# Kernel optimization log

Measured on AMD Instinct MI355X. Metric: run time of the kernel, lower is better.

## Reference

```python
import jax, jax.numpy as jnp
import numpy as np

TEMPERATURE = 8.0  # sqrt(head_dim=64)
MASK_FILL = -1e9


def setup_inputs() -> dict:
    key = jax.random.key(0)
    kq, kk, kv, km = jax.random.split(key, 4)
    B, H, S, D = 4, 16, 2048, 64
    q = jax.random.normal(kq, (B, H, S, D), dtype=jnp.float32)
    k = jax.random.normal(kk, (B, H, S, D), dtype=jnp.float32)
    v = jax.random.normal(kv, (B, H, S, D), dtype=jnp.float32)
    mask = jax.random.randint(km, (B, 1, S, S), 0, 2).astype(bool)
    return {"q": q, "k": k, "v": v, "mask": mask}


def reference(q, k, v, mask):
    # scores: [B,H,S,S]
    attn = jnp.einsum('bhqd,bhkd->bhqk', q / TEMPERATURE, k)
    attn = jnp.where(mask, MASK_FILL, attn)
    attn = jax.nn.softmax(attn, axis=-1)  # dropout in eval mode = identity
    out = jnp.einsum('bhqk,bhkd->bhqd', attn, v)
    return (out, attn)
```

## Files before the change

kernel.cpp:

```cpp
#include <hip/hip_runtime.h>
#include <math.h>


#define SEQ 2048
#define HD 64
#define NH 16
#define NB 4

typedef float floatx4 __attribute__((ext_vector_type(4)));
typedef __bf16 bf16x8 __attribute__((ext_vector_type(8)));

__device__ __forceinline__ void split8(const float4 a, const float4 b, const float s,
                                       bf16x8& hi, bf16x8& lo) {
  float f[8] = {a.x * s, a.y * s, a.z * s, a.w * s,
                b.x * s, b.y * s, b.z * s, b.w * s};
#pragma unroll
  for (int j = 0; j < 8; ++j) {
    __bf16 h = (__bf16)f[j];
    hi[j] = h;
    lo[j] = (__bf16)(f[j] - (float)h);
  }
}

__global__ __launch_bounds__(256, 2) void sdpa_kernel(
    const float* __restrict__ qp, const float* __restrict__ kp,
    const float* __restrict__ vp, const int* __restrict__ maskp,
    float* __restrict__ outp) {
  const int tid  = threadIdx.x;
  const int lane = tid & 63;
  const int w    = tid >> 6;
  const int ll   = lane & 15;
  const int quad = lane >> 4;
  const int q0   = blockIdx.x * 16;
  const int bh   = blockIdx.y;
  const int b    = bh >> 4;

  __shared__ __align__(16) __bf16 vT[64][264];
  __shared__ __align__(16) __bf16 pC[16][264];
  __shared__ float red_m[4][16];
  __shared__ float red_l[4][16];

  const size_t bh_off = (size_t)bh * (SEQ * HD);

  bf16x8 qhi0, qlo0, qhi1, qlo1;
  {
    const float* qr = qp + bh_off + (size_t)(q0 + ll) * HD + quad * 8;
    float4 a0 = *(const float4*)(qr);
    float4 a1 = *(const float4*)(qr + 4);
    float4 a2 = *(const float4*)(qr + 32);
    float4 a3 = *(const float4*)(qr + 36);
    split8(a0, a1, 0.125f, qhi0, qlo0);
    split8(a2, a3, 0.125f, qhi1, qlo1);
  }

  floatx4 acc[32];
#pragma unroll
  for (int i = 0; i < 32; ++i) acc[i] = 0.f;

  const float* kb = kp + bh_off;
#pragma unroll
  for (int i = 0; i < 32; ++i) {
    const int col0 = (4 * i + w) * 16;
    const float* kr = kb + (size_t)(col0 + ll) * HD + quad * 8;
    float4 a0 = *(const float4*)(kr);
    float4 a1 = *(const float4*)(kr + 4);
    float4 a2 = *(const float4*)(kr + 32);
    float4 a3 = *(const float4*)(kr + 36);
    bf16x8 khi0, klo0, khi1, klo1;
    split8(a0, a1, 1.f, khi0, klo0);
    split8(a2, a3, 1.f, khi1, klo1);
    floatx4 t = acc[i];
    t = __builtin_amdgcn_mfma_f32_16x16x32_bf16(qhi0, khi0, t, 0, 0, 0);
    t = __builtin_amdgcn_mfma_f32_16x16x32_bf16(qlo0, khi0, t, 0, 0, 0);
    t = __builtin_amdgcn_mfma_f32_16x16x32_bf16(qhi0, klo0, t, 0, 0, 0);
    t = __builtin_amdgcn_mfma_f32_16x16x32_bf16(qhi1, khi1, t, 0, 0, 0);
    t = __builtin_amdgcn_mfma_f32_16x16x32_bf16(qlo1, khi1, t, 0, 0, 0);
    t = __builtin_amdgcn_mfma_f32_16x16x32_bf16(qhi1, klo1, t, 0, 0, 0);
    acc[i] = t;
  }

  const int* mb = maskp + (size_t)b * SEQ * SEQ;
  float mx[4] = {-INFINITY, -INFINITY, -INFINITY, -INFINITY};
#pragma unroll
  for (int i = 0; i < 32; ++i) {
    const int col = (4 * i + w) * 16 + ll;
#pragma unroll
    for (int r = 0; r < 4; ++r) {
      const int row = q0 + quad * 4 + r;
      const int mv = mb[(size_t)row * SEQ + col];
      float sv = mv ? -1e9f : acc[i][r];
      acc[i][r] = sv;
      mx[r] = fmaxf(mx[r], sv);
    }
  }
#pragma unroll
  for (int d = 1; d < 16; d <<= 1) {
#pragma unroll
    for (int r = 0; r < 4; ++r) mx[r] = fmaxf(mx[r], __shfl_xor(mx[r], d, 64));
  }
  if (ll == 0) {
#pragma unroll
    for (int r = 0; r < 4; ++r) red_m[w][quad * 4 + r] = mx[r];
  }
  __syncthreads();
  float mrow[4];
#pragma unroll
  for (int r = 0; r < 4; ++r) {
    const int row = quad * 4 + r;
    mrow[r] = fmaxf(fmaxf(red_m[0][row], red_m[1][row]),
                    fmaxf(red_m[2][row], red_m[3][row]));
  }

  float sm[4] = {0.f, 0.f, 0.f, 0.f};
#pragma unroll
  for (int i = 0; i < 32; ++i) {
#pragma unroll
    for (int r = 0; r < 4; ++r) {
      float e = __expf(acc[i][r] - mrow[r]);
      acc[i][r] = e;
      sm[r] += e;
    }
  }
#pragma unroll
  for (int d = 1; d < 16; d <<= 1) {
#pragma unroll
    for (int r = 0; r < 4; ++r) sm[r] += __shfl_xor(sm[r], d, 64);
  }
  if (ll == 0) {
#pragma unroll
    for (int r = 0; r < 4; ++r) red_l[w][quad * 4 + r] = sm[r];
  }
  __syncthreads();
  float linv[4];
#pragma unroll
  for (int r = 0; r < 4; ++r) {
    const int row = quad * 4 + r;
    linv[r] = 1.0f / (red_l[0][row] + red_l[1][row] + red_l[2][row] + red_l[3][row]);
  }

  float* attn = outp + (size_t)(NB * NH * SEQ * HD) + (size_t)bh * SEQ * SEQ;
#pragma unroll
  for (int i = 0; i < 32; ++i) {
    const int col = (4 * i + w) * 16 + ll;
#pragma unroll
    for (int r = 0; r < 4; ++r) {
      const int row = q0 + quad * 4 + r;
      float p = acc[i][r] * linv[r];
      acc[i][r] = p;
      attn[(size_t)row * SEQ + col] = p;
    }
  }

  floatx4 oacc = 0.f;
  const float* vb = vp + bh_off;
#pragma unroll
  for (int c = 0; c < 8; ++c) {
    {
      const float* vr = vb + (size_t)(c * 256 + tid) * HD;
#pragma unroll
      for (int d4 = 0; d4 < 16; ++d4) {
        float4 vv = *(const float4*)(vr + d4 * 4);
        vT[d4 * 4 + 0][tid] = (__bf16)vv.x;
        vT[d4 * 4 + 1][tid] = (__bf16)vv.y;
        vT[d4 * 4 + 2][tid] = (__bf16)vv.z;
        vT[d4 * 4 + 3][tid] = (__bf16)vv.w;
      }
    }
#pragma unroll
    for (int u = 0; u < 4; ++u) {
      const int lt = w + 4 * u;
#pragma unroll
      for (int r = 0; r < 4; ++r)
        pC[quad * 4 + r][lt * 16 + ll] = (__bf16)acc[4 * c + u][r];
    }
    __syncthreads();
#pragma unroll
    for (int kk = 0; kk < 8; ++kk) {
      bf16x8 af = *(const bf16x8*)&pC[ll][kk * 32 + quad * 8];
      bf16x8 bf = *(const bf16x8*)&vT[w * 16 + ll][kk * 32 + quad * 8];
      oacc = __builtin_amdgcn_mfma_f32_16x16x32_bf16(af, bf, oacc, 0, 0, 0);
    }
    __syncthreads();
  }

  float* ob = outp + bh_off + (size_t)q0 * HD;
#pragma unroll
  for (int r = 0; r < 4; ++r)
    ob[(size_t)(quad * 4 + r) * HD + w * 16 + ll] = oacc[r];
}

extern "C" void kernel_launch(void* const* d_in, const int* in_sizes, int n_in,
                              void* d_out, int out_size, void* d_ws, size_t ws_size,
                              hipStream_t stream) {
  const float* q = (const float*)d_in[0];
  const float* k = (const float*)d_in[1];
  const float* v = (const float*)d_in[2];
  const int* mask = (const int*)d_in[3];
  float* out = (float*)d_out;
  dim3 grid(SEQ / 16, NB * NH);
  sdpa_kernel<<<grid, dim3(256), 0, stream>>>(q, k, v, mask, out);
}
```

Before: 2.230 ms.

## Precompute split-bf16 K, transposed V and bitpacked mask in workspace, two-pass softmax

Adds prep kernels that split K into bf16 hi/lo halves, transpose V to bf16 in workspace, and pack the int mask into bit words. The main kernel then runs an online max/sum pass and a second pass that recomputes QK, writes the attention probabilities with nontemporal stores and feeds them into the PV MFMAs through lane shuffles instead of LDS. The intent is to stop every query block from re-converting K/V and re-reading the 16M-int mask. The cost is three extra launches, double the QK compute, and a fallback path when the workspace is too small.

```diff
diff --git a/kernel.cpp b/kernel.cpp
--- a/kernel.cpp
+++ b/kernel.cpp
@@ -6,6 +6,11 @@
 #define HD 64
 #define NH 16
 #define NB 4
+#define BHN (NB * NH)
+#define KN ((size_t)BHN * SEQ * HD)
+#define MASK_FILL -1e9f
+#define QSCALE (0.125f * 1.44269504088896f)
+#define WS_REQUIRED (3 * KN * sizeof(__bf16) + (size_t)NB * 64 * SEQ * sizeof(unsigned))
 
 typedef float floatx4 __attribute__((ext_vector_type(4)));
 typedef __bf16 bf16x8 __attribute__((ext_vector_type(8)));
@@ -22,7 +27,245 @@
   }
 }
 
-__global__ __launch_bounds__(256, 2) void sdpa_kernel(
+__device__ __forceinline__ unsigned pkbf(float a, float b) {
+  union { __bf16 h[2]; unsigned u; } x;
+  x.h[0] = (__bf16)a;
+  x.h[1] = (__bf16)b;
+  return x.u;
+}
+
+
+__global__ void prep_splitk(const float* __restrict__ kp, __bf16* __restrict__ khi,
+                            __bf16* __restrict__ klo) {
+  size_t i = ((size_t)blockIdx.x * 256 + threadIdx.x) * 8;
+  float4 a = *(const float4*)(kp + i);
+  float4 b = *(const float4*)(kp + i + 4);
+  bf16x8 hi, lo;
+  float f[8] = {a.x, a.y, a.z, a.w, b.x, b.y, b.z, b.w};
+#pragma unroll
+  for (int j = 0; j < 8; ++j) {
+    __bf16 h = (__bf16)f[j];
+    hi[j] = h;
+    lo[j] = (__bf16)(f[j] - (float)h);
+  }
+  *(bf16x8*)(khi + i) = hi;
+  *(bf16x8*)(klo + i) = lo;
+}
+
+__global__ void prep_vt(const float* __restrict__ vp, __bf16* __restrict__ vT) {
+  __shared__ __bf16 tile[64][72];
+  const int bhi = blockIdx.x >> 5;
+  const int s0 = (blockIdx.x & 31) * 64;
+  const int t = threadIdx.x;
+  const float* vb = vp + (size_t)bhi * SEQ * HD + (size_t)s0 * HD;
+#pragma unroll
+  for (int c = 0; c < 4; ++c) {
+    int ft = c * 256 + t;
+    int sl = ft >> 4, d0 = (ft & 15) * 4;
+    float4 x = *(const float4*)(vb + (size_t)sl * HD + d0);
+    tile[sl][d0 + 0] = (__bf16)x.x;
+    tile[sl][d0 + 1] = (__bf16)x.y;
+    tile[sl][d0 + 2] = (__bf16)x.z;
+    tile[sl][d0 + 3] = (__bf16)x.w;
+  }
+  __syncthreads();
+  const int d = t >> 2, sc = (t & 3) * 16;
+  __bf16* o = vT + (size_t)bhi * HD * SEQ + (size_t)d * SEQ + s0 + sc;
+  bf16x8 v0, v1;
+#pragma unroll
+  for (int j = 0; j < 8; ++j) {
+    v0[j] = tile[sc + j][d];
+    v1[j] = tile[sc + 8 + j][d];
+  }
+  *(bf16x8*)o = v0;
+  *(bf16x8*)(o + 8) = v1;
+}
+
+__global__ void prep_mask(const int* __restrict__ mp, unsigned* __restrict__ mbT) {
+  const int lane = threadIdx.x & 63;
+  const int w = threadIdx.x >> 6;
+  const size_t g0 = ((size_t)blockIdx.x * 4 + w) * 64;
+  unsigned long long bits = __ballot(mp[g0 + lane] != 0);
+  if (lane == 0) {
+    const int b = (int)(g0 / ((size_t)SEQ * SEQ));
+    const size_t rem = g0 % ((size_t)SEQ * SEQ);
+    const int row = (int)(rem / SEQ);
+    const int c = (int)(rem % SEQ) >> 5;
+    mbT[((size_t)b * 64 + c) * SEQ + row] = (unsigned)bits;
+    mbT[((size_t)b * 64 + c + 1) * SEQ + row] = (unsigned)(bits >> 32);
+  }
+}
+
+
+struct TileOut { unsigned d0, d1; };
+
+__device__ __forceinline__ TileOut do_tile(const __bf16* __restrict__ kh,
+                                           const __bf16* __restrict__ kl,
+                                           bf16x8 qhi0, bf16x8 qlo0, bf16x8 qhi1,
+                                           bf16x8 qlo1, unsigned bits4, float mf,
+                                           float linv, float* attn_addr) {
+  bf16x8 kh0 = *(const bf16x8*)kh, kh1 = *(const bf16x8*)(kh + 32);
+  bf16x8 kl0 = *(const bf16x8*)kl, kl1 = *(const bf16x8*)(kl + 32);
+  floatx4 a = 0.f;
+  a = __builtin_amdgcn_mfma_f32_16x16x32_bf16(kh0, qhi0, a, 0, 0, 0);
+  a = __builtin_amdgcn_mfma_f32_16x16x32_bf16(kl0, qhi0, a, 0, 0, 0);
+  a = __builtin_amdgcn_mfma_f32_16x16x32_bf16(kh0, qlo0, a, 0, 0, 0);
+  a = __builtin_amdgcn_mfma_f32_16x16x32_bf16(kh1, qhi1, a, 0, 0, 0);
+  a = __builtin_amdgcn_mfma_f32_16x16x32_bf16(kl1, qhi1, a, 0, 0, 0);
+  a = __builtin_amdgcn_mfma_f32_16x16x32_bf16(kh1, qlo1, a, 0, 0, 0);
+  float s0 = (bits4 & 1u) ? MASK_FILL : a[0];
+  float s1 = (bits4 & 2u) ? MASK_FILL : a[1];
+  float s2 = (bits4 & 4u) ? MASK_FILL : a[2];
+  float s3 = (bits4 & 8u) ? MASK_FILL : a[3];
+  float p0 = exp2f(s0 - mf) * linv;
+  float p1 = exp2f(s1 - mf) * linv;
+  float p2 = exp2f(s2 - mf) * linv;
+  float p3 = exp2f(s3 - mf) * linv;
+  floatx4 st = {p0, p1, p2, p3};
+  __builtin_nontemporal_store(st, (floatx4*)attn_addr);
+  TileOut o;
+  o.d0 = pkbf(p0, p1);
+  o.d1 = pkbf(p2, p3);
+  return o;
+}
+
+__global__ __launch_bounds__(256, 4) void sdpa_main(
+    const float* __restrict__ qp, const __bf16* __restrict__ khi,
+    const __bf16* __restrict__ klo, const __bf16* __restrict__ vT,
+    const unsigned* __restrict__ mbT, float* __restrict__ outp) {
+  const int tid = threadIdx.x;
+  const int lane = tid & 63;
+  const int w = tid >> 6;
+  const int ll = lane & 15;
+  const int quad = lane >> 4;
+  const int q0 = blockIdx.x * 16;
+  const int bh = blockIdx.y;
+  const int b = bh >> 4;
+
+  __shared__ float red_m[4][16];
+  __shared__ float red_l[4][16];
+  __shared__ float outred[4][64][17];
+
+  const size_t bh_off = (size_t)bh * (SEQ * HD);
+
+  bf16x8 qhi0, qlo0, qhi1, qlo1;
+  {
+    const float* qr = qp + bh_off + (size_t)(q0 + ll) * HD + quad * 8;
+    split8(*(const float4*)(qr), *(const float4*)(qr + 4), QSCALE, qhi0, qlo0);
+    split8(*(const float4*)(qr + 32), *(const float4*)(qr + 36), QSCALE, qhi1, qlo1);
+  }
+
+  const unsigned* mrow = mbT + (size_t)b * 64 * SEQ + (q0 + ll);
+
+  float m = -INFINITY, l = 0.f;
+#pragma unroll 4
+  for (int i = 0; i < 32; ++i) {
+    const int t = w * 32 + i;
+    const size_t kb = bh_off + (size_t)(t * 16 + ll) * HD + quad * 8;
+    bf16x8 kh0 = *(const bf16x8*)(khi + kb), kh1 = *(const bf16x8*)(khi + kb + 32);
+    bf16x8 kl0 = *(const bf16x8*)(klo + kb), kl1 = *(const bf16x8*)(klo + kb + 32);
+    floatx4 a = 0.f;
+    a = __builtin_amdgcn_mfma_f32_16x16x32_bf16(kh0, qhi0, a, 0, 0, 0);
+    a = __builtin_amdgcn_mfma_f32_16x16x32_bf16(kl0, qhi0, a, 0, 0, 0);
+    a = __builtin_amdgcn_mfma_f32_16x16x32_bf16(kh0, qlo0, a, 0, 0, 0);
+    a = __builtin_amdgcn_mfma_f32_16x16x32_bf16(kh1, qhi1, a, 0, 0, 0);
+    a = __builtin_amdgcn_mfma_f32_16x16x32_bf16(kl1, qhi1, a, 0, 0, 0);
+    a = __builtin_amdgcn_mfma_f32_16x16x32_bf16(kh1, qlo1, a, 0, 0, 0);
+    const unsigned bits = mrow[(size_t)(t >> 1) * SEQ] >> ((t & 1) * 16 + quad * 4);
+    float s0 = (bits & 1u) ? MASK_FILL : a[0];
+    float s1 = (bits & 2u) ? MASK_FILL : a[1];
+    float s2 = (bits & 4u) ? MASK_FILL : a[2];
+    float s3 = (bits & 8u) ? MASK_FILL : a[3];
+    float tm = fmaxf(fmaxf(s0, s1), fmaxf(s2, s3));
+    float mn = fmaxf(m, tm);
+    l = l * exp2f(m - mn) +
+        ((exp2f(s0 - mn) + exp2f(s1 - mn)) + (exp2f(s2 - mn) + exp2f(s3 - mn)));
+    m = mn;
+  }
+#pragma unroll
+  for (int d = 16; d <= 32; d <<= 1) {
+    float mo = __shfl_xor(m, d, 64);
+    float lo_ = __shfl_xor(l, d, 64);
+    float mn = fmaxf(m, mo);
+    l = l * exp2f(m - mn) + lo_ * exp2f(mo - mn);
+    m = mn;
+  }
+  if (lane < 16) {
+    red_m[w][lane] = m;
+    red_l[w][lane] = l;
+  }
+  __syncthreads();
+  float mf = fmaxf(fmaxf(red_m[0][ll], red_m[1][ll]),
+                   fmaxf(red_m[2][ll], red_m[3][ll]));
+  float lf = red_l[0][ll] * exp2f(red_m[0][ll] - mf) +
+             red_l[1][ll] * exp2f(red_m[1][ll] - mf) +
+             red_l[2][ll] * exp2f(red_m[2][ll] - mf) +
+             red_l[3][ll] * exp2f(red_m[3][ll] - mf);
+  const float linv = 1.0f / lf;
+
+  floatx4 o0 = 0.f, o1 = 0.f, o2 = 0.f, o3 = 0.f;
+  float* attnrow = outp + (size_t)(BHN * SEQ * HD) + (size_t)bh * SEQ * SEQ +
+                   (size_t)(q0 + ll) * SEQ;
+  const __bf16* vb = vT + (size_t)bh * HD * SEQ;
+  for (int i2 = 0; i2 < 16; ++i2) {
+    const int tA = w * 32 + 2 * i2;
+    const int j0 = tA * 16;
+    const unsigned bits = mrow[(size_t)(tA >> 1) * SEQ];
+    const size_t kbA = bh_off + (size_t)(tA * 16 + ll) * HD + quad * 8;
+    const size_t kbB = kbA + (size_t)16 * HD;
+    TileOut A = do_tile(khi + kbA, klo + kbA, qhi0, qlo0, qhi1, qlo1,
+                        bits >> (quad * 4), mf, linv, attnrow + j0 + quad * 4);
+    TileOut B = do_tile(khi + kbB, klo + kbB, qhi0, qlo0, qhi1, qlo1,
+                        bits >> (16 + quad * 4), mf, linv,
+                        attnrow + j0 + 16 + quad * 4);
+    unsigned dw0 = A.d0, dw1 = A.d1, dw2 = B.d0, dw3 = B.d1;
+    unsigned u0 = __shfl_xor(dw0, 16, 64), u1 = __shfl_xor(dw1, 16, 64);
+    unsigned u2 = __shfl_xor(dw2, 16, 64), u3 = __shfl_xor(dw3, 16, 64);
+    const bool qodd = (quad & 1);
+    unsigned lo0 = qodd ? u0 : dw0, lo1 = qodd ? u1 : dw1;
+    unsigned lo2 = qodd ? dw0 : u0, lo3 = qodd ? dw1 : u1;
+    unsigned hi0 = qodd ? u2 : dw2, hi1 = qodd ? u3 : dw3;
+    unsigned hi2 = qodd ? dw2 : u2, hi3 = qodd ? dw3 : u3;
+    const bool qlo2 = (quad < 2);
+    unsigned s0 = qlo2 ? hi0 : lo0, s1 = qlo2 ? hi1 : lo1;
+    unsigned s2 = qlo2 ? hi2 : lo2, s3 = qlo2 ? hi3 : lo3;
+    unsigned r0 = __shfl_xor(s0, 32, 64), r1 = __shfl_xor(s1, 32, 64);
+    unsigned r2 = __shfl_xor(s2, 32, 64), r3 = __shfl_xor(s3, 32, 64);
+    union { unsigned u[4]; bf16x8 v; } pf;
+    pf.u[0] = (quad == 0) ? lo0 : (quad == 3) ? hi0 : r0;
+    pf.u[1] = (quad == 0) ? lo1 : (quad == 3) ? hi1 : r1;
+    pf.u[2] = (quad == 0) ? lo2 : (quad == 3) ? hi2 : r2;
+    pf.u[3] = (quad == 0) ? lo3 : (quad == 3) ? hi3 : r3;
+    const __bf16* vr = vb + (size_t)ll * SEQ + j0 + quad * 8;
+    o0 = __builtin_amdgcn_mfma_f32_16x16x32_bf16(*(const bf16x8*)(vr), pf.v, o0, 0, 0, 0);
+    o1 = __builtin_amdgcn_mfma_f32_16x16x32_bf16(*(const bf16x8*)(vr + 16 * SEQ), pf.v, o1, 0, 0, 0);
+    o2 = __builtin_amdgcn_mfma_f32_16x16x32_bf16(*(const bf16x8*)(vr + 32 * SEQ), pf.v, o2, 0, 0, 0);
+    o3 = __builtin_amdgcn_mfma_f32_16x16x32_bf16(*(const bf16x8*)(vr + 48 * SEQ), pf.v, o3, 0, 0, 0);
+  }
+
+#pragma unroll
+  for (int r = 0; r < 4; ++r) {
+    outred[w][ 0 + quad * 4 + r][ll] = o0[r];
+    outred[w][16 + quad * 4 + r][ll] = o1[r];
+    outred[w][32 + quad * 4 + r][ll] = o2[r];
+    outred[w][48 + quad * 4 + r][ll] = o3[r];
+  }
+  __syncthreads();
+  {
+    const int qq = tid >> 4;
+    const int d0 = (tid & 15) * 4;
+    floatx4 res;
+#pragma unroll
+    for (int j = 0; j < 4; ++j)
+      res[j] = outred[0][d0 + j][qq] + outred[1][d0 + j][qq] +
+               outred[2][d0 + j][qq] + outred[3][d0 + j][qq];
+    __builtin_nontemporal_store(
+        res, (floatx4*)(outp + bh_off + (size_t)(q0 + qq) * HD + d0));
+  }
+}
+
+
+__global__ __launch_bounds__(256, 2) void sdpa_fallback(
     const float* __restrict__ qp, const float* __restrict__ kp,
     const float* __restrict__ vp, const int* __restrict__ maskp,
     float* __restrict__ outp) {
@@ -197,6 +440,20 @@
   const float* v = (const float*)d_in[2];
   const int* mask = (const int*)d_in[3];
   float* out = (float*)d_out;
-  dim3 grid(SEQ / 16, NB * NH);
-  sdpa_kernel<<<grid, dim3(256), 0, stream>>>(q, k, v, mask, out);
-}
+
+  if (ws_size < WS_REQUIRED || d_ws == nullptr) {
+    dim3 grid(SEQ / 16, NB * NH);
+    sdpa_fallback<<<grid, dim3(256), 0, stream>>>(q, k, v, mask, out);
+    return;
+  }
+
+  __bf16* khi = (__bf16*)d_ws;
+  __bf16* klo = khi + KN;
+  __bf16* vT = klo + KN;
+  unsigned* mbT = (unsigned*)(vT + KN);
+
+  prep_splitk<<<4096, 256, 0, stream>>>(k, khi, klo);
+  prep_vt<<<2048, 256, 0, stream>>>(v, vT);
+  prep_mask<<<65536, 256, 0, stream>>>(mask, mbT);
+  sdpa_main<<<dim3(SEQ / 16, BHN), dim3(256), 0, stream>>>(q, khi, klo, vT, mbT, out);
+}
```

After: 2.191 ms. About the same (-1.8%).
